# Performance work log

Hardware: AMD Instinct MI355X
Metric: run time of the kernel (lower is better)

## Reference

```python
import jax, jax.numpy as jnp
import numpy as np

S, B, D, H = 2048, 2, 1024, 16
DK = D // H  # 64
SCALE = 1.0 / np.sqrt(DK)


def setup_inputs() -> dict:
    key = jax.random.key(0)
    ks = jax.random.split(key, 12)
    std = 0.02
    return {
        "query": jax.random.normal(ks[0], (S, B, D), jnp.float32),
        "key": jax.random.normal(ks[1], (S, B, D), jnp.float32),
        "value": jax.random.normal(ks[2], (S, B, D), jnp.float32),
        "wq": jax.random.normal(ks[3], (D, D), jnp.float32) * std,
        "bq": jnp.zeros((D,), jnp.float32),
        "wk": jax.random.normal(ks[4], (D, D), jnp.float32) * std,
        "bk": jnp.zeros((D,), jnp.float32),
        "wv": jax.random.normal(ks[5], (D, D), jnp.float32) * std,
        "bv": jnp.zeros((D,), jnp.float32),
        "wo": jax.random.normal(ks[6], (D, D), jnp.float32) * std,
        "bo": jnp.zeros((D,), jnp.float32),
    }


def _proj(x, w, b):
    # (s, b, d_model) -> (s, b, heads, d_k); nn.Linear uses x @ W^T + b
    y = x @ w.T + b
    return y.reshape(*x.shape[:-1], H, DK)


def reference(query, key, value, wq, bq, wk, bk, wv, bv, wo, bo):
    q = _proj(query, wq, bq)   # (s, b, h, d)
    k = _proj(key, wk, bk)
    v = _proj(value, wv, bv)
    scores = jnp.einsum("ibhd,jbhd->ijbh", q, k) * SCALE  # (s_q, s_k, b, h)
    attn = jax.nn.softmax(scores, axis=1)  # softmax over key axis (dim=1)
    # dropout is identity in eval/reference mode
    x = jnp.einsum("ijbh,jbhd->ibhd", attn, v)  # (s, b, h, d)
    x = x.reshape(S, B, D)
    return x @ wo.T + bo
```

## Files before the change

kernel.cpp:

```cpp
#include <hip/hip_runtime.h>
#include <hip/hip_bf16.h>

namespace {

constexpr int SEQ = 2048;
constexpr int NB  = 2;
constexpr int DM  = 1024;
constexpr int NHD = 16;
constexpr int DKH = 64;
constexpr int MROWS = SEQ * NB;
constexpr float SM_SCALE_L2E = 0.125f * 1.44269504088896340736f;
constexpr size_t HT = (size_t)NB * NHD * SEQ * DKH;

typedef short bf16x8 __attribute__((ext_vector_type(8)));
typedef short bf16x4 __attribute__((ext_vector_type(4)));
typedef float f32x4  __attribute__((ext_vector_type(4)));

__device__ inline short f2bf(float f) {
    __hip_bfloat16 h = __float2bfloat16(f);
    return *reinterpret_cast<short*>(&h);
}

__device__ inline unsigned perm_pack_bf16(float hi, float lo) {
    return __builtin_amdgcn_perm(__float_as_uint(hi), __float_as_uint(lo),
                                 0x07060302u);
}

__device__ inline float fexp2(float x) {
#if __has_builtin(__builtin_amdgcn_exp2f)
    return __builtin_amdgcn_exp2f(x);
#else
    return exp2f(x);
#endif
}

__device__ inline void gload_lds16(const short* g, short* l) {
    __builtin_amdgcn_global_load_lds(
        (const __attribute__((address_space(1))) void*)g,
        (__attribute__((address_space(3))) void*)l, 16, 0, 0);
}

__global__ __launch_bounds__(256)
void cast_all(const float* __restrict__ q, const float* __restrict__ k,
              const float* __restrict__ v, const float* __restrict__ w0,
              const float* __restrict__ w1, const float* __restrict__ w2,
              const float* __restrict__ w3, short* __restrict__ oq,
              short* __restrict__ ok, short* __restrict__ ov,
              short* __restrict__ ow)
{
    const int y = blockIdx.y;
    const float* s;
    short* d;
    if (y < 3) {
        s = y == 0 ? q : y == 1 ? k : v;
        d = y == 0 ? oq : y == 1 ? ok : ov;
    } else {
        if (blockIdx.x >= 512) return;
        s = y == 3 ? w0 : y == 4 ? w1 : y == 5 ? w2 : w3;
        d = ow + (size_t)(y - 3) * (DM * DM);
    }
    const size_t t = (size_t)blockIdx.x * 256 + threadIdx.x;
    const float4 a = ((const float4*)s)[2 * t];
    const float4 b = ((const float4*)s)[2 * t + 1];
    short r[8] = {f2bf(a.x), f2bf(a.y), f2bf(a.z), f2bf(a.w),
                  f2bf(b.x), f2bf(b.y), f2bf(b.z), f2bf(b.w)};
    *(bf16x8*)(d + 8 * t) = *(bf16x8*)r;
}

__global__ __launch_bounds__(256)
void gemm_qkv(const short* __restrict__ X0, const short* __restrict__ X1,
              const short* __restrict__ X2, const short* __restrict__ W,
              const float* __restrict__ b0, const float* __restrict__ b1,
              const float* __restrict__ b2, short* __restrict__ Qb,
              short* __restrict__ Kb, short* __restrict__ Vt)
{
    __shared__ short sAB[2][8192];
    const int tid  = threadIdx.x;
    const int lane = tid & 63;
    const int wave = tid >> 6;
    const int i16  = lane & 15;
    const int quad = lane >> 4;

    const int c    = blockIdx.y * gridDim.x + blockIdx.x;
    const int xcd  = c & 7;
    const int idx  = c >> 3;
    const int m0   = (xcd * 4 + (idx & 3)) * 128;
    const int n0g  = (idx >> 2) * 128;

    const int R0   = (wave & 1) * 64;
    const int C0   = (wave >> 1) * 64;

    const int seg = n0g >> 10;
    const short* X = seg == 0 ? X0 : seg == 1 ? X1 : X2;

    const int rl = lane >> 2;
    const int sl = (lane & 3) ^ ((rl & 6) >> 1);

    const short* ag[2]; int alo[2];
    const short* bg[2]; int blo[2];
    #pragma unroll
    for (int i = 0; i < 2; ++i) {
        const int row = i * 64 + wave * 16 + rl;
        ag[i] = X + (size_t)(m0 + row) * DM + sl * 8;
        alo[i] = i * 2048 + wave * 512;
        bg[i] = W + (size_t)(n0g + row) * DM + sl * 8;
        blo[i] = 4096 + i * 2048 + wave * 512;
    }

    const int rsw = (quad ^ ((i16 & 6) >> 1)) * 8;
    int aoff[4], boff[4];
    #pragma unroll
    for (int rt = 0; rt < 4; ++rt)
        aoff[rt] = (R0 + rt * 16 + i16) * 32 + rsw;
    #pragma unroll
    for (int ct = 0; ct < 4; ++ct)
        boff[ct] = 4096 + (C0 + ct * 16 + i16) * 32 + rsw;

    f32x4 acc[4][4];
    #pragma unroll
    for (int rt = 0; rt < 4; ++rt)
        #pragma unroll
        for (int ct = 0; ct < 4; ++ct) acc[rt][ct] = (f32x4){0.f, 0.f, 0.f, 0.f};

    #pragma unroll
    for (int i = 0; i < 2; ++i) gload_lds16(ag[i], &sAB[0][alo[i]]);
    #pragma unroll
    for (int i = 0; i < 2; ++i) gload_lds16(bg[i], &sAB[0][blo[i]]);
    #pragma unroll
    for (int i = 0; i < 2; ++i) { ag[i] += 32; bg[i] += 32; }
    __syncthreads();

    for (int ks = 0; ks < 32; ++ks) {
        const int p = ks & 1;
        if (ks < 31) {
            #pragma unroll
            for (int i = 0; i < 2; ++i) gload_lds16(ag[i], &sAB[1 - p][alo[i]]);
            #pragma unroll
            for (int i = 0; i < 2; ++i) gload_lds16(bg[i], &sAB[1 - p][blo[i]]);
            #pragma unroll
            for (int i = 0; i < 2; ++i) { ag[i] += 32; bg[i] += 32; }
        }
        const short* buf = sAB[p];
        bf16x8 af[4], bfr[4];
        #pragma unroll
        for (int rt = 0; rt < 4; ++rt) af[rt] = *(const bf16x8*)&buf[aoff[rt]];
        #pragma unroll
        for (int ct = 0; ct < 4; ++ct) bfr[ct] = *(const bf16x8*)&buf[boff[ct]];
        #pragma unroll
        for (int rt = 0; rt < 4; ++rt)
            #pragma unroll
            for (int ct = 0; ct < 4; ++ct)
                acc[rt][ct] = __builtin_amdgcn_mfma_f32_16x16x32_bf16(
                    af[rt], bfr[ct], acc[rt][ct], 0, 0, 0);
        __syncthreads();
    }

    #pragma unroll
    for (int ct = 0; ct < 4; ++ct) {
        const int n = n0g + C0 + ct * 16 + i16;
        const int nn  = n & 1023;
        const int h = nn >> 6, dk = nn & 63;
        const float* bp = seg == 0 ? b0 : seg == 1 ? b1 : b2;
        const float bb = bp[nn];
        const float sc = seg == 0 ? SM_SCALE_L2E : 1.0f;
        #pragma unroll
        for (int rt = 0; rt < 4; ++rt)
            #pragma unroll
            for (int r = 0; r < 4; ++r) {
                const int m = m0 + R0 + rt * 16 + quad * 4 + r;
                const int s = m >> 1, b = m & 1;
                const short val = f2bf((acc[rt][ct][r] + bb) * sc);
                if (seg == 2) {
                    const int sp = (s & ~31) | (((s >> 2) & 3) << 3) |
                                   (((s >> 4) & 1) << 2) | (s & 3);
                    Vt[(((size_t)(b * NHD + h) * DKH + dk) << 11) + sp] = val;
                } else {
                    short* dst = seg == 0 ? Qb : Kb;
                    dst[((size_t)(b * NHD + h) * SEQ + s) * DKH + dk] = val;
                }
            }
    }
}

__global__ __launch_bounds__(256)
void gemm_out(const short* __restrict__ X, const short* __restrict__ W,
              const float* __restrict__ bias, float* __restrict__ Y)
{
    __shared__ short sAB[2][12288];
    const int tid  = threadIdx.x;
    const int lane = tid & 63;
    const int wave = tid >> 6;
    const int i16  = lane & 15;
    const int quad = lane >> 4;

    const int c   = blockIdx.y * gridDim.x + blockIdx.x;
    const int xcd = c & 7;
    const int idx = c >> 3;
    const int m0  = (xcd * 4 + (idx & 3)) * 128;
    const int n0  = (idx >> 2) * 64;

    const int R0   = wave * 32;

    const int srow = lane >> 3;
    const int ssl  = (lane & 7) ^ srow;

    const short* ag[4]; int alo[4];
    const short* bg[2]; int blo[2];
    #pragma unroll
    for (int i = 0; i < 4; ++i) {
        const int row = i * 32 + wave * 8 + srow;
        ag[i] = X + (size_t)(m0 + row) * DM + ssl * 8;
        alo[i] = i * 2048 + wave * 512;
    }
    #pragma unroll
    for (int i = 0; i < 2; ++i) {
        const int row = i * 32 + wave * 8 + srow;
        bg[i] = W + (size_t)(n0 + row) * DM + ssl * 8;
        blo[i] = 8192 + i * 2048 + wave * 512;
    }

    int aoff[2][2], boff[4][2];
    #pragma unroll
    for (int rt = 0; rt < 2; ++rt)
        #pragma unroll
        for (int kc = 0; kc < 2; ++kc)
            aoff[rt][kc] = (R0 + rt * 16 + i16) * 64 +
                           (((kc * 4 + quad) ^ (i16 & 7)) * 8);
    #pragma unroll
    for (int ct = 0; ct < 4; ++ct)
        #pragma unroll
        for (int kc = 0; kc < 2; ++kc)
            boff[ct][kc] = 8192 + (ct * 16 + i16) * 64 +
                           (((kc * 4 + quad) ^ (i16 & 7)) * 8);

    f32x4 acc[2][4];
    #pragma unroll
    for (int rt = 0; rt < 2; ++rt)
        #pragma unroll
        for (int ct = 0; ct < 4; ++ct) acc[rt][ct] = (f32x4){0.f, 0.f, 0.f, 0.f};

    #pragma unroll
    for (int i = 0; i < 4; ++i) gload_lds16(ag[i], &sAB[0][alo[i]]);
    #pragma unroll
    for (int i = 0; i < 2; ++i) gload_lds16(bg[i], &sAB[0][blo[i]]);
    #pragma unroll
    for (int i = 0; i < 4; ++i) ag[i] += 64;
    #pragma unroll
    for (int i = 0; i < 2; ++i) bg[i] += 64;
    __syncthreads();

    for (int ks = 0; ks < 16; ++ks) {
        const int p = ks & 1;
        if (ks < 15) {
            #pragma unroll
            for (int i = 0; i < 4; ++i) gload_lds16(ag[i], &sAB[1 - p][alo[i]]);
            #pragma unroll
            for (int i = 0; i < 2; ++i) gload_lds16(bg[i], &sAB[1 - p][blo[i]]);
            #pragma unroll
            for (int i = 0; i < 4; ++i) ag[i] += 64;
            #pragma unroll
            for (int i = 0; i < 2; ++i) bg[i] += 64;
        }
        const short* buf = sAB[p];
        #pragma unroll
        for (int kc = 0; kc < 2; ++kc) {
            bf16x8 af[2], bfr[4];
            #pragma unroll
            for (int rt = 0; rt < 2; ++rt) af[rt] = *(const bf16x8*)&buf[aoff[rt][kc]];
            #pragma unroll
            for (int ct = 0; ct < 4; ++ct) bfr[ct] = *(const bf16x8*)&buf[boff[ct][kc]];
            #pragma unroll
            for (int rt = 0; rt < 2; ++rt)
                #pragma unroll
                for (int ct = 0; ct < 4; ++ct)
                    acc[rt][ct] = __builtin_amdgcn_mfma_f32_16x16x32_bf16(
                        af[rt], bfr[ct], acc[rt][ct], 0, 0, 0);
        }
        __syncthreads();
    }

    #pragma unroll
    for (int ct = 0; ct < 4; ++ct) {
        const int n = n0 + ct * 16 + i16;
        const float bb = bias[n];
        #pragma unroll
        for (int rt = 0; rt < 2; ++rt)
            #pragma unroll
            for (int r = 0; r < 4; ++r) {
                const int m = m0 + R0 + rt * 16 + quad * 4 + r;
                Y[(size_t)m * DM + n] = acc[rt][ct][r] + bb;
            }
    }
}

__global__ __launch_bounds__(512)
void attn_mfma4(const short* __restrict__ Qb, const short* __restrict__ Kb,
                const short* __restrict__ Vtb, short* __restrict__ Xa)
{
    __shared__ short sm[16384];

    const int tid  = threadIdx.x;
    const int lane = tid & 63;
    const int wave = tid >> 6;
    const int i16  = lane & 15;
    const int quad = lane >> 4;

    const int c   = blockIdx.y * gridDim.x + blockIdx.x;
    const int xcd = c & 7;
    const int idx = c >> 3;
    const int bh  = xcd * 4 + (idx & 3);
    const int r0  = (idx >> 2) * 256;

    bf16x8 qf[2][2];
    #pragma unroll
    for (int qt = 0; qt < 2; ++qt) {
        const short* qrow =
            Qb + ((size_t)bh * SEQ + r0 + wave * 32 + qt * 16 + i16) * DKH;
        qf[qt][0] = *(const bf16x8*)(qrow + quad * 8);
        qf[qt][1] = *(const bf16x8*)(qrow + 32 + quad * 8);
    }

    bf16x8 vone;
    #pragma unroll
    for (int i = 0; i < 8; ++i) vone[i] = (short)0x3F80;

    f32x4 o[2][4], ol[2];
    #pragma unroll
    for (int qt = 0; qt < 2; ++qt) {
        #pragma unroll
        for (int dkt = 0; dkt < 4; ++dkt) o[qt][dkt] = (f32x4){0.f, 0.f, 0.f, 0.f};
        ol[qt] = (f32x4){0.f, 0.f, 0.f, 0.f};
    }

    const int srow = lane >> 3;
    const int ssl  = (lane & 7) ^ srow;
    const short* kg = Kb  + (size_t)bh * SEQ * DKH +
                      (size_t)(wave * 8 + srow) * DKH + ssl * 8;
    const short* vg = Vtb + (size_t)bh * DKH * SEQ +
                      (size_t)(wave * 8 + srow) * SEQ + ssl * 8;
    const int kls = wave * 512;
    const int vls = 4096 + wave * 512;

    int koff[4][2];
    #pragma unroll
    for (int t = 0; t < 4; ++t)
        #pragma unroll
        for (int kc = 0; kc < 2; ++kc)
            koff[t][kc] = (t * 16 + i16) * 64 +
                          (((kc * 4 + quad) ^ (i16 & 7)) * 8);
    int voff2[2][4];
    #pragma unroll
    for (int u = 0; u < 2; ++u)
        #pragma unroll
        for (int dkt = 0; dkt < 4; ++dkt)
            voff2[u][dkt] = 4096 + (dkt * 16 + i16) * 64 +
                            (((u * 4 + quad) ^ (i16 & 7)) * 8);

    gload_lds16(kg, &sm[kls]);
    gload_lds16(vg, &sm[vls]);
    __syncthreads();

    for (int jt = 0; jt < 32; ++jt) {
        const int p = jt & 1;
        if (jt < 31) {
            const int bo = (1 - p) * 8192;
            gload_lds16(kg + (size_t)(jt + 1) * 64 * DKH, &sm[bo + kls]);
            gload_lds16(vg + (jt + 1) * 64, &sm[bo + vls]);
        }
        const short* buf = sm + p * 8192;

        bf16x8 kf[4][2];
        #pragma unroll
        for (int t = 0; t < 4; ++t) {
            kf[t][0] = *(const bf16x8*)&buf[koff[t][0]];
            kf[t][1] = *(const bf16x8*)&buf[koff[t][1]];
        }

        bf16x4 pa[2][4];
        #pragma unroll
        for (int qt = 0; qt < 2; ++qt) {
            #pragma unroll
            for (int t = 0; t < 4; ++t) {
                f32x4 st = (f32x4){0.f, 0.f, 0.f, 0.f};
                st = __builtin_amdgcn_mfma_f32_16x16x32_bf16(kf[t][0], qf[qt][0], st, 0, 0, 0);
                st = __builtin_amdgcn_mfma_f32_16x16x32_bf16(kf[t][1], qf[qt][1], st, 0, 0, 0);
                const float e0 = fexp2(st[0]);
                const float e1 = fexp2(st[1]);
                const float e2 = fexp2(st[2]);
                const float e3 = fexp2(st[3]);
                union { unsigned u[2]; bf16x4 v; } pk;
                pk.u[0] = perm_pack_bf16(e1, e0);
                pk.u[1] = perm_pack_bf16(e3, e2);
                pa[qt][t] = pk.v;
            }
        }

        #pragma unroll
        for (int u = 0; u < 2; ++u) {
            const bf16x8 a0 = __builtin_shufflevector(
                pa[0][2 * u], pa[0][2 * u + 1], 0, 1, 2, 3, 4, 5, 6, 7);
            const bf16x8 a1 = __builtin_shufflevector(
                pa[1][2 * u], pa[1][2 * u + 1], 0, 1, 2, 3, 4, 5, 6, 7);
            #pragma unroll
            for (int dkt = 0; dkt < 4; ++dkt) {
                const bf16x8 vb = *(const bf16x8*)&buf[voff2[u][dkt]];
                o[0][dkt] = __builtin_amdgcn_mfma_f32_16x16x32_bf16(
                    a0, vb, o[0][dkt], 0, 0, 0);
                o[1][dkt] = __builtin_amdgcn_mfma_f32_16x16x32_bf16(
                    a1, vb, o[1][dkt], 0, 0, 0);
            }
            ol[0] = __builtin_amdgcn_mfma_f32_16x16x32_bf16(a0, vone, ol[0], 0, 0, 0);
            ol[1] = __builtin_amdgcn_mfma_f32_16x16x32_bf16(a1, vone, ol[1], 0, 0, 0);
        }
        __syncthreads();
    }

    const int b = bh / NHD;
    const int h = bh % NHD;
    #pragma unroll
    for (int qt = 0; qt < 2; ++qt) {
        #pragma unroll
        for (int r = 0; r < 4; ++r) {
            const float iv = 1.f / ol[qt][r];
            const int row = wave * 32 + qt * 16 + quad * 4 + r;
            const int s = r0 + row;
            const int m = s * NB + b;
            short* op = Xa + (size_t)m * DM + h * DKH;
            #pragma unroll
            for (int dkt = 0; dkt < 4; ++dkt)
                op[dkt * 16 + i16] = f2bf(o[qt][dkt][r] * iv);
        }
    }
}

}

extern "C" void kernel_launch(void* const* d_in, const int* in_sizes, int n_in,
                              void* d_out, int out_size, void* d_ws, size_t ws_size,
                              hipStream_t stream)
{
    const float* query = (const float*)d_in[0];
    const float* key_  = (const float*)d_in[1];
    const float* value = (const float*)d_in[2];
    const float* wq    = (const float*)d_in[3];
    const float* bq    = (const float*)d_in[4];
    const float* wk    = (const float*)d_in[5];
    const float* bk    = (const float*)d_in[6];
    const float* wv    = (const float*)d_in[7];
    const float* bv    = (const float*)d_in[8];
    const float* wo    = (const float*)d_in[9];
    const float* bo    = (const float*)d_in[10];
    float* out = (float*)d_out;

    char* ws = (char*)d_ws;
    const size_t HB = HT * sizeof(short);
    short* Qb = (short*)(ws);
    short* Kb = Qb + HT;
    short* Vt = Qb + 2 * HT;
    short* Xq = (short*)(ws + 3 * HB);
    short* Xa = Xq;
    short* Xk = (short*)(ws + 4 * HB);
    short* Xv = (short*)(ws + 5 * HB);
    short* Wb = (short*)(ws + 6 * HB);

    cast_all<<<dim3(MROWS * DM / (8 * 256), 7), 256, 0, stream>>>(
        query, key_, value, wq, wk, wv, wo, Xq, Xk, Xv, Wb);

    gemm_qkv<<<dim3(MROWS / 128, 3 * DM / 128), 256, 0, stream>>>(
        Xq, Xk, Xv, Wb, bq, bk, bv, Qb, Kb, Vt);

    attn_mfma4<<<dim3(SEQ / 256, NB * NHD), 512, 0, stream>>>(Qb, Kb, Vt, Xa);

    gemm_out<<<dim3(MROWS / 128, DM / 64), 256, 0, stream>>>(
        Xa, Wb + 3 * (size_t)DM * DM, bo, out);
}
```

Baseline: 201.4 us.

## Triple-buffer QKV GEMM LDS staging with partial waitcnt and split MFMA phases

Moves the QKV projection GEMM from double to triple buffering in LDS, so two k-slices are in flight while one is consumed. It waits with vmcnt(4) rather than a full drain. The MFMA block is split into two halves separated by a barrier, and s_setprio is raised around the MFMA issue to interleave waves. LDS use grows by half, which may lower occupancy. The hand-written waitcnt and barrier placement must stay correct for every buffer reuse.

Measured after the change: 205.0 us. Within noise of the previous version (+1.8%).

```diff
diff --git a/kernel.cpp b/kernel.cpp
--- a/kernel.cpp
+++ b/kernel.cpp
@@ -74,7 +74,7 @@
               const float* __restrict__ b2, short* __restrict__ Qb,
               short* __restrict__ Kb, short* __restrict__ Vt)
 {
-    __shared__ short sAB[2][8192];
+    __shared__ short sAB[3][8192];
     const int tid  = threadIdx.x;
     const int lane = tid & 63;
     const int wave = tid >> 6;
@@ -122,37 +122,57 @@
         #pragma unroll
         for (int ct = 0; ct < 4; ++ct) acc[rt][ct] = (f32x4){0.f, 0.f, 0.f, 0.f};
 
-    #pragma unroll
-    for (int i = 0; i < 2; ++i) gload_lds16(ag[i], &sAB[0][alo[i]]);
-    #pragma unroll
-    for (int i = 0; i < 2; ++i) gload_lds16(bg[i], &sAB[0][blo[i]]);
-    #pragma unroll
-    for (int i = 0; i < 2; ++i) { ag[i] += 32; bg[i] += 32; }
-    __syncthreads();
+    auto stage_into = [&](short* base) {
+        gload_lds16(ag[0], base + alo[0]);
+        gload_lds16(ag[1], base + alo[1]);
+        gload_lds16(bg[0], base + blo[0]);
+        gload_lds16(bg[1], base + blo[1]);
+        ag[0] += 32; ag[1] += 32; bg[0] += 32; bg[1] += 32;
+    };
+
+    stage_into(sAB[0]);
+    stage_into(sAB[1]);
+    asm volatile("s_waitcnt vmcnt(4)" ::: "memory");
+    __builtin_amdgcn_s_barrier();
 
     for (int ks = 0; ks < 32; ++ks) {
-        const int p = ks & 1;
-        if (ks < 31) {
-            #pragma unroll
-            for (int i = 0; i < 2; ++i) gload_lds16(ag[i], &sAB[1 - p][alo[i]]);
-            #pragma unroll
-            for (int i = 0; i < 2; ++i) gload_lds16(bg[i], &sAB[1 - p][blo[i]]);
-            #pragma unroll
-            for (int i = 0; i < 2; ++i) { ag[i] += 32; bg[i] += 32; }
-        }
-        const short* buf = sAB[p];
+        if (ks < 30) stage_into(sAB[(ks + 2) % 3]);
+        const short* buf = sAB[ks % 3];
+
         bf16x8 af[4], bfr[4];
         #pragma unroll
         for (int rt = 0; rt < 4; ++rt) af[rt] = *(const bf16x8*)&buf[aoff[rt]];
         #pragma unroll
-        for (int ct = 0; ct < 4; ++ct) bfr[ct] = *(const bf16x8*)&buf[boff[ct]];
+        for (int ct = 0; ct < 2; ++ct) bfr[ct] = *(const bf16x8*)&buf[boff[ct]];
+        __builtin_amdgcn_s_setprio(1);
         #pragma unroll
         for (int rt = 0; rt < 4; ++rt)
             #pragma unroll
-            for (int ct = 0; ct < 4; ++ct)
+            for (int ct = 0; ct < 2; ++ct)
                 acc[rt][ct] = __builtin_amdgcn_mfma_f32_16x16x32_bf16(
                     af[rt], bfr[ct], acc[rt][ct], 0, 0, 0);
-        __syncthreads();
+        __builtin_amdgcn_s_setprio(0);
+        __builtin_amdgcn_s_barrier();
+
+        #pragma unroll
+        for (int ct = 2; ct < 4; ++ct) bfr[ct] = *(const bf16x8*)&buf[boff[ct]];
+        __builtin_amdgcn_s_setprio(1);
+        #pragma unroll
+        for (int rt = 0; rt < 4; ++rt)
+            #pragma unroll
+            for (int ct = 2; ct < 4; ++ct)
+                acc[rt][ct] = __builtin_amdgcn_mfma_f32_16x16x32_bf16(
+                    af[rt], bfr[ct], acc[rt][ct], 0, 0, 0);
+        __builtin_amdgcn_s_setprio(0);
+
+        if (ks < 31) {
+            if (ks < 30) {
+                asm volatile("s_waitcnt vmcnt(4)" ::: "memory");
+            } else {
+                asm volatile("s_waitcnt vmcnt(0)" ::: "memory");
+            }
+            __builtin_amdgcn_s_barrier();
+        }
     }
 
     #pragma unroll
```

## Load QKV GEMM A operand directly from global into registers, bypassing LDS

Applied to the files above, without the earlier changes.

The QKV projection GEMM no longer stages the activation (A) tile through shared memory. Each lane now loads its A fragments straight from global memory into registers, prefetching the next k-step while the current MFMAs run. Only the weight (B) tile stays double-buffered in LDS, which halves LDS use and removes the A-side LDS reads. In exchange, A rows shared by the two column-waves are fetched twice from global or L2, each load is a 16-byte per-lane access spread across rows, and register pressure rises from the prefetch buffers and the fully unrolled k-loop.

Result: slower. 222.9 us (+10.7%).

```diff
diff --git a/kernel.cpp b/kernel.cpp
--- a/kernel.cpp
+++ b/kernel.cpp
@@ -74,7 +74,7 @@
               const float* __restrict__ b2, short* __restrict__ Qb,
               short* __restrict__ Kb, short* __restrict__ Vt)
 {
-    __shared__ short sAB[2][8192];
+    __shared__ short Bs[2][4096];
     const int tid  = threadIdx.x;
     const int lane = tid & 63;
     const int wave = tid >> 6;
@@ -96,54 +96,51 @@
     const int rl = lane >> 2;
     const int sl = (lane & 3) ^ ((rl & 6) >> 1);
 
-    const short* ag[2]; int alo[2];
     const short* bg[2]; int blo[2];
     #pragma unroll
     for (int i = 0; i < 2; ++i) {
         const int row = i * 64 + wave * 16 + rl;
-        ag[i] = X + (size_t)(m0 + row) * DM + sl * 8;
-        alo[i] = i * 2048 + wave * 512;
         bg[i] = W + (size_t)(n0g + row) * DM + sl * 8;
-        blo[i] = 4096 + i * 2048 + wave * 512;
-    }
+        blo[i] = i * 2048 + wave * 512;
+    }
+
+    const short* aptr[4];
+    #pragma unroll
+    for (int rt = 0; rt < 4; ++rt)
+        aptr[rt] = X + (size_t)(m0 + R0 + rt * 16 + i16) * DM + quad * 8;
 
     const int rsw = (quad ^ ((i16 & 6) >> 1)) * 8;
-    int aoff[4], boff[4];
+    int boff[4];
+    #pragma unroll
+    for (int ct = 0; ct < 4; ++ct)
+        boff[ct] = (C0 + ct * 16 + i16) * 32 + rsw;
+
+    f32x4 acc[4][4];
     #pragma unroll
     for (int rt = 0; rt < 4; ++rt)
-        aoff[rt] = (R0 + rt * 16 + i16) * 32 + rsw;
-    #pragma unroll
-    for (int ct = 0; ct < 4; ++ct)
-        boff[ct] = 4096 + (C0 + ct * 16 + i16) * 32 + rsw;
-
-    f32x4 acc[4][4];
-    #pragma unroll
-    for (int rt = 0; rt < 4; ++rt)
         #pragma unroll
         for (int ct = 0; ct < 4; ++ct) acc[rt][ct] = (f32x4){0.f, 0.f, 0.f, 0.f};
 
     #pragma unroll
-    for (int i = 0; i < 2; ++i) gload_lds16(ag[i], &sAB[0][alo[i]]);
-    #pragma unroll
-    for (int i = 0; i < 2; ++i) gload_lds16(bg[i], &sAB[0][blo[i]]);
-    #pragma unroll
-    for (int i = 0; i < 2; ++i) { ag[i] += 32; bg[i] += 32; }
+    for (int i = 0; i < 2; ++i) gload_lds16(bg[i], &Bs[0][blo[i]]);
+    bf16x8 af[4];
+    #pragma unroll
+    for (int rt = 0; rt < 4; ++rt) af[rt] = *(const bf16x8*)(aptr[rt]);
     __syncthreads();
 
+    #pragma unroll
     for (int ks = 0; ks < 32; ++ks) {
         const int p = ks & 1;
+        bf16x8 afn[4];
         if (ks < 31) {
-            #pragma unroll
-            for (int i = 0; i < 2; ++i) gload_lds16(ag[i], &sAB[1 - p][alo[i]]);
-            #pragma unroll
-            for (int i = 0; i < 2; ++i) gload_lds16(bg[i], &sAB[1 - p][blo[i]]);
-            #pragma unroll
-            for (int i = 0; i < 2; ++i) { ag[i] += 32; bg[i] += 32; }
-        }
-        const short* buf = sAB[p];
-        bf16x8 af[4], bfr[4];
-        #pragma unroll
-        for (int rt = 0; rt < 4; ++rt) af[rt] = *(const bf16x8*)&buf[aoff[rt]];
+            gload_lds16(bg[0] + (ks + 1) * 32, &Bs[1 - p][blo[0]]);
+            gload_lds16(bg[1] + (ks + 1) * 32, &Bs[1 - p][blo[1]]);
+            #pragma unroll
+            for (int rt = 0; rt < 4; ++rt)
+                afn[rt] = *(const bf16x8*)(aptr[rt] + (ks + 1) * 32);
+        }
+        const short* buf = Bs[p];
+        bf16x8 bfr[4];
         #pragma unroll
         for (int ct = 0; ct < 4; ++ct) bfr[ct] = *(const bf16x8*)&buf[boff[ct]];
         #pragma unroll
@@ -152,6 +149,10 @@
             for (int ct = 0; ct < 4; ++ct)
                 acc[rt][ct] = __builtin_amdgcn_mfma_f32_16x16x32_bf16(
                     af[rt], bfr[ct], acc[rt][ct], 0, 0, 0);
+        if (ks < 31) {
+            #pragma unroll
+            for (int rt = 0; rt < 4; ++rt) af[rt] = afn[rt];
+        }
         __syncthreads();
     }
 
```
